# Kernel tuning notes

Hardware: AMD Instinct MI355X
Metric: run time of the kernel (lower is better)

Reference implementation:

```python
import jax, jax.numpy as jnp
import numpy as np

B, N, D, H, DH, F, L, LC = 32, 256, 512, 8, 64, 2048, 8, 2
NEG = -1e9
SCALE = 1.0 / float(np.sqrt(DH))


def _ln(x, g, b, eps=1e-3):
    # keras LayerNormalization default epsilon=1e-3
    m = jnp.mean(x, -1, keepdims=True)
    v = jnp.mean((x - m) ** 2, -1, keepdims=True)
    return (x - m) * jax.lax.rsqrt(v + eps) * g + b


def setup_inputs() -> dict:
    key = jax.random.key(0)
    ks = jax.random.split(key, 20)
    n = lambda k, s: jax.random.normal(k, s, dtype=jnp.float32) * 0.02
    lengths = jax.random.randint(ks[0], (B,), N // 2, N + 1)
    mask = jnp.arange(N)[None, :] < lengths[:, None]  # [B,N] bool
    return {
        'x': jax.random.normal(ks[1], (B, N, D), dtype=jnp.float32),
        'interaction': jax.random.normal(ks[2], (B, N, N, H), dtype=jnp.float32) * 0.1,
        'class_token': n(ks[3], (1, 1, D)),
        'p_ln1_g': jnp.ones((L, D)), 'p_ln1_b': jnp.zeros((L, D)),
        'p_wq': n(ks[4], (L, D, D)), 'p_wk': n(ks[5], (L, D, D)),
        'p_wv': n(ks[6], (L, D, D)), 'p_wo': n(ks[7], (L, D, D)),
        'p_ln2_g': jnp.ones((L, D)), 'p_ln2_b': jnp.zeros((L, D)),
        'p_w1': n(ks[8], (L, D, F)), 'p_b1': jnp.zeros((L, F)),
        'p_w2': n(ks[9], (L, F, D)), 'p_b2': jnp.zeros((L, D)),
        'c_ln1_g': jnp.ones((LC, D)), 'c_ln1_b': jnp.zeros((LC, D)),
        'c_qk': n(ks[10], (LC, D, H, DH)), 'c_qb': jnp.zeros((LC, H, DH)),
        'c_kk': n(ks[11], (LC, D, H, DH)), 'c_kb': jnp.zeros((LC, H, DH)),
        'c_vk': n(ks[12], (LC, D, H, DH)), 'c_vb': jnp.zeros((LC, H, DH)),
        'c_ok': n(ks[13], (LC, H, DH, D)), 'c_ob': jnp.zeros((LC, D)),
        'c_ln2_g': jnp.ones((LC, D)), 'c_ln2_b': jnp.zeros((LC, D)),
        'c_w1': n(ks[14], (LC, D, F)), 'c_b1': jnp.zeros((LC, F)),
        'c_w2': n(ks[15], (LC, F, D)), 'c_b2': jnp.zeros((LC, D)),
        'mask': mask,
    }


def _part_forward(x, interaction, class_token, p_ln1_g, p_ln1_b, p_wq, p_wk, p_wv, p_wo,
                  p_ln2_g, p_ln2_b, p_w1, p_b1, p_w2, p_b2,
                  c_ln1_g, c_ln1_b, c_qk, c_qb, c_kk, c_kb, c_vk, c_vb, c_ok, c_ob,
                  c_ln2_g, c_ln2_b, c_w1, c_b1, c_w2, c_b2, mask):
    # pairwise particle mask [B,1,N,N]; keras Softmax adds (1-mask)*-1e9
    pmask = (mask[:, None, None, :] & mask[:, None, :, None]).astype(x.dtype)
    padd = (1.0 - pmask) * NEG
    inter = jnp.transpose(interaction, (0, 3, 1, 2))  # [B,H,N,N]
    h = x
    for i in range(L):
        # pre-LN interaction self-attention (dropout inactive at inference)
        hn = _ln(h, p_ln1_g[i], p_ln1_b[i])
        q = (hn @ p_wq[i]).reshape(B, N, H, DH)
        k = (hn @ p_wk[i]).reshape(B, N, H, DH)
        v = (hn @ p_wv[i]).reshape(B, N, H, DH)
        s = jnp.einsum('bqhd,bkhd->bhqk', q, k) * SCALE + inter + padd
        a = jax.nn.softmax(s, axis=-1)
        o = jnp.einsum('bhqk,bkhd->bqhd', a, v).reshape(B, N, D) @ p_wo[i]
        h = h + o
        # pre-LN FFN, gelu (exact, tf.nn.gelu default)
        fn = _ln(h, p_ln2_g[i], p_ln2_b[i])
        h = h + (jax.nn.gelu(fn @ p_w1[i] + p_b1[i], approximate=False) @ p_w2[i] + p_b2[i])
    query = jnp.broadcast_to(class_token, (B, 1, D)).astype(x.dtype)
    cmask = jnp.concatenate([jnp.ones((B, 1), bool), mask], axis=1)[:, None, None, :].astype(x.dtype)
    cadd = (1.0 - cmask) * NEG  # [B,1,1,N+1]
    for i in range(LC):
        # class-attention: K/V from LN(concat([token, particles])), Q from RAW token (as in source)
        cat = jnp.concatenate([query, h], axis=1)  # [B,N+1,D]
        cn = _ln(cat, c_ln1_g[i], c_ln1_b[i])
        qh = jnp.einsum('bqd,dhk->bqhk', query, c_qk[i]) + c_qb[i]
        kh = jnp.einsum('bsd,dhk->bshk', cn, c_kk[i]) + c_kb[i]
        vh = jnp.einsum('bsd,dhk->bshk', cn, c_vk[i]) + c_vb[i]
        s = jnp.einsum('bqhk,bshk->bhqs', qh, kh) * SCALE + cadd
        a = jax.nn.softmax(s, axis=-1)
        o = jnp.einsum('bhqs,bshk->bqhk', a, vh)
        o = jnp.einsum('bqhk,hkd->bqd', o, c_ok[i]) + c_ob[i]
        query = query + o
        fn = _ln(query, c_ln2_g[i], c_ln2_b[i])
        query = query + (jax.nn.gelu(fn @ c_w1[i] + c_b1[i], approximate=False) @ c_w2[i] + c_b2[i])
    return query  # [B,1,D]


def reference(x, interaction, class_token, p_ln1_g, p_ln1_b, p_wq, p_wk, p_wv, p_wo,
              p_ln2_g, p_ln2_b, p_w1, p_b1, p_w2, p_b2,
              c_ln1_g, c_ln1_b, c_qk, c_qb, c_kk, c_kb, c_vk, c_vb, c_ok, c_ob,
              c_ln2_g, c_ln2_b, c_w1, c_b1, c_w2, c_b2, mask):
    return _part_forward(x, interaction, class_token, p_ln1_g, p_ln1_b, p_wq, p_wk, p_wv, p_wo,
                         p_ln2_g, p_ln2_b, p_w1, p_b1, p_w2, p_b2,
                         c_ln1_g, c_ln1_b, c_qk, c_qb, c_kk, c_kb, c_vk, c_vb, c_ok, c_ob,
                         c_ln2_g, c_ln2_b, c_w1, c_b1, c_w2, c_b2, mask)
```

## Files before the change

kernel.cpp:

```cpp
#include <hip/hip_runtime.h>
#include <hip/hip_fp16.h>

#define B_ 32
#define N_ 256
#define D_ 512
#define H_ 8
#define DH_ 64
#define F_ 2048
#define L_ 8
#define LC_ 2
#define NEG_ (-1e9f)
#define SCALE_ 0.125f
#define LDSK 72
#define KCH_ 128

typedef unsigned short u16;
typedef unsigned int u32;
typedef long long s64;
typedef __attribute__((ext_vector_type(8))) short bf16x8;
typedef __attribute__((ext_vector_type(8))) unsigned short u16x8;
typedef __attribute__((ext_vector_type(4))) float f32x4;

__device__ __forceinline__ float b2f(u16 u) {
    union { u32 i; float f; } v; v.i = ((u32)u) << 16; return v.f;
}
__device__ __forceinline__ u16 f2b(float f) {
    union { float f; u32 i; } v; v.f = f;
    u32 x = v.i;
    u32 r = (x + 0x7FFFu + ((x >> 16) & 1u)) >> 16;
    return (u16)r;
}
__device__ __forceinline__ float h2f(u16 u) {
    __half_raw hr; hr.x = u;
    return __half2float(__half(hr));
}
__device__ __forceinline__ void gld16(u16* lds, const u16* g) {
    __builtin_amdgcn_global_load_lds(
        (const __attribute__((address_space(1))) u16*)g,
        (__attribute__((address_space(3))) u16*)lds, 16, 0, 0);
}
__device__ __forceinline__ float ldf(const void* p, size_t i, int fl) {
    if (fl == 1) return ((const float*)p)[i];
    if (fl == 0) return b2f(((const u16*)p)[i]);
    return h2f(((const u16*)p)[i]);
}
__device__ __forceinline__ void ld4(const void* p, size_t i, int fl, float o[4]) {
    if (fl == 1) {
        const float4 v = *(const float4*)((const float*)p + i);
        o[0] = v.x; o[1] = v.y; o[2] = v.z; o[3] = v.w;
    } else if (fl == 0) {
        const ushort4 v = *(const ushort4*)((const u16*)p + i);
        o[0] = b2f(v.x); o[1] = b2f(v.y); o[2] = b2f(v.z); o[3] = b2f(v.w);
    } else {
        const ushort4 v = *(const ushort4*)((const u16*)p + i);
        o[0] = h2f(v.x); o[1] = h2f(v.y); o[2] = h2f(v.z); o[3] = h2f(v.w);
    }
}

__global__ void sniff_kernel(const u32* __restrict__ g1, int* __restrict__ flag) {
    if (threadIdx.x == 0 && blockIdx.x == 0) {
        u32 w = g1[0];
        int f = 0;
        if (w == 0x3F800000u) f = 1;
        else if (w == 0x3C003C00u) f = 2;
        flag[0] = f;
    }
}

__global__ void mask_decode_kernel(const unsigned char* __restrict__ raw,
                                   float* __restrict__ mf) {
    int i = blockIdx.x * 256 + threadIdx.x;
    if (i >= B_ * N_) return;
    unsigned char c0 = raw[0], c1 = raw[1], c4 = raw[4];
    bool v;
    if (c1 == 0x3F || c1 == 0x3C) {
        v = ((const u16*)raw)[i] != 0;
    } else if (c0 == 1 && c1 == 1) {
        v = raw[i] != 0;
    } else if (c0 == 1 && c1 == 0) {
        if (c4 == 1) v = ((const int*)raw)[i] != 0;
        else v = ((const long long*)raw)[i] != 0;
    } else {
        v = ((const float*)raw)[i] != 0.0f;
    }
    mf[i] = v ? 1.0f : 0.0f;
}

__global__ void cvt_in_kernel(const void* __restrict__ in, float* __restrict__ out,
                              int n, const int* __restrict__ fl) {
    int i = blockIdx.x * 256 + threadIdx.x;
    if (i < n) out[i] = ldf(in, (size_t)i, fl[0]);
}
__global__ void bcast_token_kernel(const void* __restrict__ ct, float* __restrict__ qry,
                                   const int* __restrict__ fl) {
    int i = blockIdx.x * 256 + threadIdx.x;
    qry[i] = ldf(ct, (size_t)(i & (D_ - 1)), fl[0]);
}
__global__ void out_copy_kernel(const float* __restrict__ in, float* __restrict__ out, int n) {
    int i = blockIdx.x * 256 + threadIdx.x;
    if (i < n) out[i] = in[i];
}
__global__ void concat_bias_kernel(const void* __restrict__ b1, s64 o1,
                                   const void* __restrict__ b2, s64 o2,
                                   float* __restrict__ dst, const int* __restrict__ flp) {
    int i = blockIdx.x * 256 + threadIdx.x;
    if (i < 512) dst[i] = ldf(b1, (size_t)(o1 + i), flp[0]);
    else if (i < 1024) dst[i] = ldf(b2, (size_t)(o2 + i - 512), flp[0]);
}

__global__ __launch_bounds__(256) void inter_t_kernel(const void* __restrict__ inter,
                                                      const float* __restrict__ mf,
                                                      u16* __restrict__ out,
                                                      const int* __restrict__ flp) {
    __shared__ float tile[256][9];
    __shared__ float mks[256];
    int fl = flp[0];
    int bq = blockIdx.x;
    int b = bq >> 8, q = bq & 255;
    int t = threadIdx.x;
    size_t base = (size_t)bq * 2048;
#pragma unroll
    for (int p = 0; p < 8; ++p) {
        int e = p * 256 + t;
        tile[e >> 3][e & 7] = ldf(inter, base + e, fl);
    }
    mks[t] = mf[b * 256 + t];
    __syncthreads();
    float mq = mf[b * 256 + q];
    int h = t >> 5;
    int k0 = (t & 31) * 8;
    u16x8 v8;
#pragma unroll
    for (int ii = 0; ii < 8; ++ii) {
        int k = k0 + ii;
        float v = tile[k][h];
        if (mq * mks[k] < 0.5f) v += NEG_;
        v8[ii] = (short)f2b(v);
    }
    *(u16x8*)(out + (((size_t)(b * 8 + h) * 256 + q) * 256 + k0)) = v8;
}

__global__ __launch_bounds__(256) void transpose_w_kernel(const void* __restrict__ W, s64 weoff,
                                                          int Nst, int Kd,
                                                          u16* __restrict__ wt,
                                                          const int* __restrict__ flp) {
    __shared__ float tile[32][33];
    int fl = flp[0];
    int n0 = blockIdx.x * 32, k0 = blockIdx.y * 32;
    int tr = threadIdx.x >> 5, tc = threadIdx.x & 31;
#pragma unroll
    for (int p = 0; p < 4; ++p) {
        int kk = p * 8 + tr;
        tile[kk][tc] = ldf(W, (size_t)(weoff + (s64)(k0 + kk) * Nst + n0 + tc), fl);
    }
    __syncthreads();
#pragma unroll
    for (int p = 0; p < 4; ++p) {
        int nn = p * 8 + tr;
        wt[(s64)(n0 + nn) * Kd + k0 + tc] = f2b(tile[tc][nn]);
    }
}

__global__ __launch_bounds__(256) void twt6_kernel(const void* __restrict__ wq,
                                                   const void* __restrict__ wk,
                                                   const void* __restrict__ wv,
                                                   const void* __restrict__ wo,
                                                   const void* __restrict__ w1,
                                                   const void* __restrict__ w2,
                                                   s64 off44, s64 offw1, s64 offw2,
                                                   u16* __restrict__ wtqkv,
                                                   u16* __restrict__ wto,
                                                   u16* __restrict__ wt1,
                                                   u16* __restrict__ wt2,
                                                   const int* __restrict__ flp) {
    __shared__ float tile[32][33];
    int fl = flp[0];
    int bid = blockIdx.x;
    const void* W; s64 weoff; int Nst, Kd; u16* dst; int lb;
    if (bid < 256)       { W = wq; weoff = off44; Nst = 512;  Kd = 512;  dst = wtqkv;          lb = bid; }
    else if (bid < 512)  { W = wk; weoff = off44; Nst = 512;  Kd = 512;  dst = wtqkv + 262144; lb = bid - 256; }
    else if (bid < 768)  { W = wv; weoff = off44; Nst = 512;  Kd = 512;  dst = wtqkv + 524288; lb = bid - 512; }
    else if (bid < 1024) { W = wo; weoff = off44; Nst = 512;  Kd = 512;  dst = wto;            lb = bid - 768; }
    else if (bid < 2048) { W = w1; weoff = offw1; Nst = 2048; Kd = 512;  dst = wt1;            lb = bid - 1024; }
    else                 { W = w2; weoff = offw2; Nst = 512;  Kd = 2048; dst = wt2;            lb = bid - 2048; }
    int nx = Nst >> 5;
    int n0 = (lb % nx) << 5, k0 = (lb / nx) << 5;
    int tr = threadIdx.x >> 5, tc = threadIdx.x & 31;
#pragma unroll
    for (int p = 0; p < 4; ++p) {
        int kk = p * 8 + tr;
        tile[kk][tc] = ldf(W, (size_t)(weoff + (s64)(k0 + kk) * Nst + n0 + tc), fl);
    }
    __syncthreads();
#pragma unroll
    for (int p = 0; p < 4; ++p) {
        int nn = p * 8 + tr;
        dst[(s64)(n0 + nn) * Kd + k0 + tc] = f2b(tile[tc][nn]);
    }
}

__global__ __launch_bounds__(256) void ln_kernel(const float* __restrict__ in,
                                                 const void* __restrict__ g,
                                                 const void* __restrict__ bta,
                                                 s64 peoff,
                                                 u16* __restrict__ out,
                                                 const int* __restrict__ flp) {
    __shared__ float ws4[4];
    __shared__ float wsq[4];
    int fl = flp[0];
    size_t row = blockIdx.x;
    int t = threadIdx.x;
    float x0 = in[row * D_ + t];
    float x1 = in[row * D_ + 256 + t];
    float s = x0 + x1;
#pragma unroll
    for (int off = 32; off > 0; off >>= 1) s += __shfl_xor(s, off);
    if ((t & 63) == 0) ws4[t >> 6] = s;
    __syncthreads();
    float mean = (ws4[0] + ws4[1] + ws4[2] + ws4[3]) * (1.0f / D_);
    float d0 = x0 - mean, d1 = x1 - mean;
    float sq = d0 * d0 + d1 * d1;
#pragma unroll
    for (int off = 32; off > 0; off >>= 1) sq += __shfl_xor(sq, off);
    if ((t & 63) == 0) wsq[t >> 6] = sq;
    __syncthreads();
    float var = (wsq[0] + wsq[1] + wsq[2] + wsq[3]) * (1.0f / D_);
    float inv = 1.0f / sqrtf(var + 1e-3f);
    out[row * D_ + t]       = f2b(d0 * inv * ldf(g, peoff + t, fl)       + ldf(bta, peoff + t, fl));
    out[row * D_ + 256 + t] = f2b(d1 * inv * ldf(g, peoff + 256 + t, fl) + ldf(bta, peoff + 256 + t, fl));
}

__global__ __launch_bounds__(256) void ln_cat_kernel(const float* __restrict__ qry,
                                                     const float* __restrict__ h,
                                                     const void* __restrict__ g,
                                                     const void* __restrict__ bta,
                                                     s64 peoff,
                                                     u16* __restrict__ out,
                                                     const int* __restrict__ flp) {
    __shared__ float ws4[4];
    __shared__ float wsq[4];
    int fl = flp[0];
    size_t row = blockIdx.x;
    int b = (int)(row / 257);
    int r = (int)(row % 257);
    const float* src = (r == 0) ? (qry + (size_t)b * D_)
                                : (h + ((size_t)b * N_ + (r - 1)) * D_);
    int t = threadIdx.x;
    float x0 = src[t];
    float x1 = src[256 + t];
    float s = x0 + x1;
#pragma unroll
    for (int off = 32; off > 0; off >>= 1) s += __shfl_xor(s, off);
    if ((t & 63) == 0) ws4[t >> 6] = s;
    __syncthreads();
    float mean = (ws4[0] + ws4[1] + ws4[2] + ws4[3]) * (1.0f / D_);
    float d0 = x0 - mean, d1 = x1 - mean;
    float sq = d0 * d0 + d1 * d1;
#pragma unroll
    for (int off = 32; off > 0; off >>= 1) sq += __shfl_xor(sq, off);
    if ((t & 63) == 0) wsq[t >> 6] = sq;
    __syncthreads();
    float var = (wsq[0] + wsq[1] + wsq[2] + wsq[3]) * (1.0f / D_);
    float inv = 1.0f / sqrtf(var + 1e-3f);
    out[row * D_ + t]       = f2b(d0 * inv * ldf(g, peoff + t, fl)       + ldf(bta, peoff + t, fl));
    out[row * D_ + 256 + t] = f2b(d1 * inv * ldf(g, peoff + 256 + t, fl) + ldf(bta, peoff + 256 + t, fl));
}

__global__ __launch_bounds__(512) void mfma_gemm_t(const u16* __restrict__ A,
                                                   const u16* __restrict__ Wt,
                                                   int wst, int wkoff,
                                                   const void* __restrict__ bias, s64 beoff,
                                                   int bflag,
                                                   const float* __restrict__ res,
                                                   void* __restrict__ C, int cbf,
                                                   int M, int N, int K, int act,
                                                   const int* __restrict__ flp) {
    __shared__ u16 Alds[2 * 128 * 64];
    __shared__ u16 Blds[2 * 128 * 64];
    int tid = threadIdx.x;
    int gx = gridDim.x;
    int nwg = gx * gridDim.y;
    int orig = blockIdx.y * gx + blockIdx.x;
    int xcd = orig & 7;
    int qq = nwg >> 3, rr = nwg & 7;
    int wg = (xcd < rr ? xcd * (qq + 1) : rr * (qq + 1) + (xcd - rr) * qq) + (orig >> 3);
    int bx = wg % gx, by = wg / gx;
    int bm = by << 7, bn = bx << 7;
    int wid = tid >> 6, lane = tid & 63;
    int wm = (wid >> 2) << 6, wn = (wid & 3) << 5;
    int l15 = lane & 15, q = lane >> 4;
    f32x4 acc[4][2];
#pragma unroll
    for (int a = 0; a < 4; ++a)
#pragma unroll
        for (int b = 0; b < 2; ++b) acc[a][b] = (f32x4){0.f, 0.f, 0.f, 0.f};
    int srow = tid >> 3;
    int sseg = tid & 7;
    int xseg = sseg ^ (srow & 7);
    const u16* arow[2];
#pragma unroll
    for (int p = 0; p < 2; ++p) {
        int gr = bm + p * 64 + srow;
        if (gr >= M) gr = M - 1;
        arow[p] = A + (size_t)gr * K + (xseg << 3);
    }
    const u16* brow[2];
#pragma unroll
    for (int p = 0; p < 2; ++p)
        brow[p] = Wt + (size_t)(bn + p * 64 + srow) * wst + wkoff + (xseg << 3);
    int dstoff = srow * 64 + (sseg << 3);
    auto stage = [&](int buf, int k0) {
        u16* Ab = Alds + buf * 8192;
        u16* Bb = Blds + buf * 8192;
#pragma unroll
        for (int p = 0; p < 2; ++p) gld16(&Ab[dstoff + p * 4096], arow[p] + k0);
#pragma unroll
        for (int p = 0; p < 2; ++p) gld16(&Bb[dstoff + p * 4096], brow[p] + k0);
    };
    int nt = K >> 6;
    stage(0, 0);
    if (nt > 1) stage(1, 64);
    for (int t = 0; t < nt; ++t) {
        if (t + 1 < nt) asm volatile("s_waitcnt vmcnt(4)" ::: "memory");
        else            asm volatile("s_waitcnt vmcnt(0)" ::: "memory");
        __builtin_amdgcn_s_barrier();
        asm volatile("" ::: "memory");
        const u16* Ac = Alds + (t & 1) * 8192;
        const u16* Bc = Blds + (t & 1) * 8192;
#pragma unroll
        for (int ks = 0; ks < 2; ++ks) {
            int seg = ((ks * 4 + q) ^ (l15 & 7)) << 3;
            bf16x8 af[4], bfr[2];
#pragma unroll
            for (int mt = 0; mt < 4; ++mt)
                af[mt] = *(const bf16x8*)(&Ac[(wm + mt * 16 + l15) * 64 + seg]);
#pragma unroll
            for (int nt2 = 0; nt2 < 2; ++nt2)
                bfr[nt2] = *(const bf16x8*)(&Bc[(wn + nt2 * 16 + l15) * 64 + seg]);
#pragma unroll
            for (int mt = 0; mt < 4; ++mt)
#pragma unroll
                for (int nt2 = 0; nt2 < 2; ++nt2)
                    acc[mt][nt2] = __builtin_amdgcn_mfma_f32_16x16x32_bf16(
                        af[mt], bfr[nt2], acc[mt][nt2], 0, 0, 0);
        }
        asm volatile("" ::: "memory");
        __builtin_amdgcn_s_barrier();
        if (t + 2 < nt) stage(t & 1, (t + 2) << 6);
    }
    int fl = (bflag >= 0) ? bflag : flp[0];
#pragma unroll
    for (int nt2 = 0; nt2 < 2; ++nt2) {
        int col = bn + wn + nt2 * 16 + l15;
        float bv = bias ? ldf(bias, (size_t)(beoff + col), fl) : 0.f;
#pragma unroll
        for (int mt = 0; mt < 4; ++mt) {
#pragma unroll
            for (int i = 0; i < 4; ++i) {
                int row = bm + wm + mt * 16 + q * 4 + i;
                if (row >= M) continue;
                float c = acc[mt][nt2][i] + bv;
                if (act) c = 0.5f * c * (1.0f + erff(c * 0.70710678118654752f));
                if (res) c += res[(size_t)row * N + col];
                if (cbf) ((u16*)C)[(size_t)row * N + col] = f2b(c);
                else     ((float*)C)[(size_t)row * N + col] = c;
            }
        }
    }
}

__global__ __launch_bounds__(256) void skinny_gemm_kernel(const void* __restrict__ A, int abf,
                                                          const void* __restrict__ W, s64 weoff,
                                                          int wst,
                                                          float* __restrict__ Cp,
                                                          int N, int K,
                                                          const int* __restrict__ flp) {
    __shared__ float As[32 * KCH_];
    int wfl = flp[0];
    int tid = threadIdx.x;
    int bn = blockIdx.x << 6;
    int ks = blockIdx.y;
    int k0 = ks * KCH_;
#pragma unroll
    for (int p = 0; p < (32 * KCH_) / 1024; ++p) {
        int idx = p * 1024 + tid * 4;
        int m = idx >> 7, c = idx & (KCH_ - 1);
        size_t gi = (size_t)m * K + k0 + c;
        if (abf) {
            const ushort4 v = *(const ushort4*)((const u16*)A + gi);
            As[idx]     = b2f(v.x);
            As[idx + 1] = b2f(v.y);
            As[idx + 2] = b2f(v.z);
            As[idx + 3] = b2f(v.w);
        } else {
            *(float4*)&As[idx] = *(const float4*)((const float*)A + gi);
        }
    }
    __syncthreads();
    int tx = tid & 63, ty = tid >> 6;
    int n = bn + tx;
    float acc[8] = {0.f, 0.f, 0.f, 0.f, 0.f, 0.f, 0.f, 0.f};
#pragma unroll 4
    for (int kk = 0; kk < KCH_; kk += 4) {
        float w0 = ldf(W, (size_t)(weoff + (s64)(k0 + kk) * wst + n), wfl);
        float w1 = ldf(W, (size_t)(weoff + (s64)(k0 + kk + 1) * wst + n), wfl);
        float w2 = ldf(W, (size_t)(weoff + (s64)(k0 + kk + 2) * wst + n), wfl);
        float w3 = ldf(W, (size_t)(weoff + (s64)(k0 + kk + 3) * wst + n), wfl);
#pragma unroll
        for (int r = 0; r < 8; ++r) {
            const float4 a = *(const float4*)&As[(ty * 8 + r) * KCH_ + kk];
            acc[r] += a.x * w0 + a.y * w1 + a.z * w2 + a.w * w3;
        }
    }
#pragma unroll
    for (int r = 0; r < 8; ++r)
        Cp[((size_t)ks * 32 + ty * 8 + r) * N + n] = acc[r];
}

__global__ __launch_bounds__(256) void skinny_epi_kernel(const float* __restrict__ Cp,
                                                         int KS, int N,
                                                         const void* __restrict__ bias, s64 beoff,
                                                         const float* __restrict__ res,
                                                         float* __restrict__ C, int act,
                                                         const int* __restrict__ flp) {
    int i = blockIdx.x * 256 + threadIdx.x;
    if (i >= 32 * N) return;
    int n = i % N;
    float s = 0.f;
    for (int ks = 0; ks < KS; ++ks) s += Cp[(size_t)ks * 32 * N + i];
    if (bias) s += ldf(bias, (size_t)(beoff + n), flp[0]);
    if (act) s = 0.5f * s * (1.0f + erff(s * 0.70710678118654752f));
    if (res) s += res[i];
    C[i] = s;
}

__global__ __launch_bounds__(256) void attn_mfma_kernel(const u16* __restrict__ QKV,
                                                        const u16* __restrict__ IT,
                                                        u16* __restrict__ O) {
    __shared__ u16 KV[256 * 72];
    __shared__ u16 Amat[64 * 264];
    int li = blockIdx.y * 4 + blockIdx.x;
    int slot = li >> 3;
    int bh = (li & 7) * 32 + (slot >> 2);
    int q0 = (slot & 3) << 6;
    int b = bh >> 3, hh = bh & 7;
    int tid = threadIdx.x;
    int w = tid >> 6, l = tid & 63, q2 = l >> 4, l15 = l & 15;
    int qrow = q0 + (w << 4) + l15;
    const u16* qptr = QKV + (size_t)(b * N_ + qrow) * 1536 + hh * DH_ + (q2 << 3);
    bf16x8 aq0 = *(const bf16x8*)(qptr);
    bf16x8 aq1 = *(const bf16x8*)(qptr + 32);
    {
        int r = tid >> 3, seg = (tid & 7) << 3;
#pragma unroll
        for (int p = 0; p < 8; ++p) {
            int k = p * 32 + r;
            *(u16x8*)(&KV[k * LDSK + seg]) =
                *(const u16x8*)(QKV + (size_t)(b * N_ + k) * 1536 + 512 + hh * DH_ + seg);
        }
    }
    u16x8 vreg[8];
    {
        const u16* vptr = QKV + (size_t)(b * N_ + (w << 6)) * 1536 + 1024 + hh * DH_ + l;
#pragma unroll
        for (int s = 0; s < 8; ++s)
#pragma unroll
            for (int e = 0; e < 8; ++e)
                vreg[s][e] = vptr[(size_t)(s * 8 + e) * 1536];
    }
    const u16* itp = IT + ((size_t)bh * N_ + q0 + (w << 4) + (q2 << 2)) * N_ + l15;
    u16 itv0[16], itv1[16], itv2[16], itv3[16];
#pragma unroll
    for (int t = 0; t < 16; ++t) {
        itv0[t] = itp[t * 16];
        itv1[t] = itp[(size_t)N_ + t * 16];
        itv2[t] = itp[(size_t)2 * N_ + t * 16];
        itv3[t] = itp[(size_t)3 * N_ + t * 16];
    }
    asm volatile("s_waitcnt lgkmcnt(0)" ::: "memory");
    __builtin_amdgcn_s_barrier();
    __builtin_amdgcn_sched_barrier(0);
    f32x4 acc[16];
#pragma unroll
    for (int t = 0; t < 16; ++t) {
        const u16* kp = &KV[(t * 16 + l15) * LDSK + (q2 << 3)];
        bf16x8 b0 = *(const bf16x8*)(kp);
        bf16x8 b1 = *(const bf16x8*)(kp + 32);
        f32x4 z = (f32x4){0.f, 0.f, 0.f, 0.f};
        z = __builtin_amdgcn_mfma_f32_16x16x32_bf16(aq0, b0, z, 0, 0, 0);
        acc[t] = __builtin_amdgcn_mfma_f32_16x16x32_bf16(aq1, b1, z, 0, 0, 0);
    }
    asm volatile("s_waitcnt lgkmcnt(0)" ::: "memory");
    __builtin_amdgcn_s_barrier();
    __builtin_amdgcn_sched_barrier(0);
#pragma unroll
    for (int s = 0; s < 8; ++s)
        *(u16x8*)(&KV[l * 264 + (w << 6) + s * 8]) = vreg[s];
    float mx[4] = {-3e38f, -3e38f, -3e38f, -3e38f};
#pragma unroll
    for (int t = 0; t < 16; ++t) {
        float s0 = acc[t][0] * SCALE_ + b2f(itv0[t]);
        float s1 = acc[t][1] * SCALE_ + b2f(itv1[t]);
        float s2 = acc[t][2] * SCALE_ + b2f(itv2[t]);
        float s3 = acc[t][3] * SCALE_ + b2f(itv3[t]);
        acc[t][0] = s0; acc[t][1] = s1; acc[t][2] = s2; acc[t][3] = s3;
        mx[0] = fmaxf(mx[0], s0);
        mx[1] = fmaxf(mx[1], s1);
        mx[2] = fmaxf(mx[2], s2);
        mx[3] = fmaxf(mx[3], s3);
    }
#pragma unroll
    for (int i = 0; i < 4; ++i) {
        mx[i] = fmaxf(mx[i], __shfl_xor(mx[i], 1));
        mx[i] = fmaxf(mx[i], __shfl_xor(mx[i], 2));
        mx[i] = fmaxf(mx[i], __shfl_xor(mx[i], 4));
        mx[i] = fmaxf(mx[i], __shfl_xor(mx[i], 8));
    }
    float sum[4] = {0.f, 0.f, 0.f, 0.f};
#pragma unroll
    for (int t = 0; t < 16; ++t)
#pragma unroll
        for (int i = 0; i < 4; ++i) {
            float e = expf(acc[t][i] - mx[i]);
            acc[t][i] = e;
            sum[i] += e;
        }
#pragma unroll
    for (int i = 0; i < 4; ++i) {
        sum[i] += __shfl_xor(sum[i], 1);
        sum[i] += __shfl_xor(sum[i], 2);
        sum[i] += __shfl_xor(sum[i], 4);
        sum[i] += __shfl_xor(sum[i], 8);
        sum[i] = 1.0f / sum[i];
    }
#pragma unroll
    for (int t = 0; t < 16; ++t)
#pragma unroll
        for (int i = 0; i < 4; ++i)
            Amat[((w << 4) + (q2 << 2) + i) * 264 + t * 16 + l15] = f2b(acc[t][i] * sum[i]);
    asm volatile("s_waitcnt lgkmcnt(0)" ::: "memory");
    __builtin_amdgcn_s_barrier();
    __builtin_amdgcn_sched_barrier(0);
    f32x4 pacc[4];
#pragma unroll
    for (int dt = 0; dt < 4; ++dt) pacc[dt] = (f32x4){0.f, 0.f, 0.f, 0.f};
#pragma unroll
    for (int kc = 0; kc < 8; ++kc) {
        bf16x8 af = *(const bf16x8*)(&Amat[((w << 4) + l15) * 264 + kc * 32 + (q2 << 3)]);
#pragma unroll
        for (int dt = 0; dt < 4; ++dt) {
            bf16x8 bf = *(const bf16x8*)(&KV[(dt * 16 + l15) * 264 + kc * 32 + (q2 << 3)]);
            pacc[dt] = __builtin_amdgcn_mfma_f32_16x16x32_bf16(af, bf, pacc[dt], 0, 0, 0);
        }
    }
    u16* ob = O + (size_t)(b * N_ + q0 + (w << 4) + (q2 << 2)) * D_ + hh * DH_ + l15;
#pragma unroll
    for (int dt = 0; dt < 4; ++dt)
#pragma unroll
        for (int i = 0; i < 4; ++i)
            ob[(size_t)i * D_ + dt * 16] = f2b(pacc[dt][i]);
}

__global__ __launch_bounds__(256) void cls_attn_kernel(const float* __restrict__ qh,
                                                       const u16* __restrict__ kvh,
                                                       const float* __restrict__ mf,
                                                       float* __restrict__ O) {
    __shared__ float qs[64];
    __shared__ float am[257];
    __shared__ float wred[4];
    __shared__ float vred[256];
    int b = blockIdx.x >> 3, hh = blockIdx.x & 7;
    int t = threadIdx.x;
    int w = t >> 6, l = t & 63;
    if (t < 64) qs[t] = qh[(size_t)b * D_ + hh * DH_ + t];
    __syncthreads();
    const u16* krow = kvh + (size_t)(b * 257 + t) * 1024 + hh * DH_;
    float s = 0.f;
#pragma unroll
    for (int seg = 0; seg < 8; ++seg) {
        u16x8 kv8 = *(const u16x8*)(krow + seg * 8);
#pragma unroll
        for (int e = 0; e < 8; ++e) s += qs[seg * 8 + e] * b2f(kv8[e]);
    }
    float cm = (t == 0) ? 1.0f : mf[b * N_ + t - 1];
    s = s * SCALE_ + ((cm > 0.5f) ? 0.0f : NEG_);
    float s256 = -1e30f;
    if (t == 0) {
        const u16* krow2 = kvh + (size_t)(b * 257 + 256) * 1024 + hh * DH_;
        float s2 = 0.f;
#pragma unroll
        for (int seg = 0; seg < 8; ++seg) {
            u16x8 kv8 = *(const u16x8*)(krow2 + seg * 8);
#pragma unroll
            for (int e = 0; e < 8; ++e) s2 += qs[seg * 8 + e] * b2f(kv8[e]);
        }
        float cm2 = mf[b * N_ + 255];
        s256 = s2 * SCALE_ + ((cm2 > 0.5f) ? 0.0f : NEG_);
    }
    float mx = (t == 0) ? fmaxf(s, s256) : s;
#pragma unroll
    for (int off = 32; off > 0; off >>= 1) mx = fmaxf(mx, __shfl_xor(mx, off));
    if (l == 0) wred[w] = mx;
    __syncthreads();
    mx = fmaxf(fmaxf(wred[0], wred[1]), fmaxf(wred[2], wred[3]));
    float p = expf(s - mx);
    float p256 = (t == 0) ? expf(s256 - mx) : 0.f;
    float sum = p + p256;
#pragma unroll
    for (int off = 32; off > 0; off >>= 1) sum += __shfl_xor(sum, off);
    __syncthreads();
    if (l == 0) wred[w] = sum;
    __syncthreads();
    float invs = 1.0f / (wred[0] + wred[1] + wred[2] + wred[3]);
    am[t] = p * invs;
    if (t == 0) am[256] = p256 * invs;
    __syncthreads();
    int g = w, d = l;
    const u16* vcol = kvh + (size_t)(b * 257 + g * 64) * 1024 + 512 + hh * DH_ + d;
    float acc = 0.f;
#pragma unroll 8
    for (int j = 0; j < 64; ++j)
        acc += am[g * 64 + j] * b2f(vcol[(size_t)j * 1024]);
    if (g == 3)
        acc += am[256] * b2f(kvh[(size_t)(b * 257 + 256) * 1024 + 512 + hh * DH_ + d]);
    vred[t] = acc;
    __syncthreads();
    if (t < 64)
        O[(size_t)b * D_ + hh * DH_ + t] = vred[t] + vred[64 + t] + vred[128 + t] + vred[192 + t];
}

extern "C" void kernel_launch(void* const* d_in, const int* in_sizes, int n_in,
                              void* d_out, int out_size, void* d_ws, size_t ws_size,
                              hipStream_t stream) {
    const void* x           = d_in[0];
    const void* interaction = d_in[1];
    const void* class_token = d_in[2];
    const void* p_ln1_g = d_in[3];
    const void* p_ln1_b = d_in[4];
    const void* p_wq    = d_in[5];
    const void* p_wk    = d_in[6];
    const void* p_wv    = d_in[7];
    const void* p_wo    = d_in[8];
    const void* p_ln2_g = d_in[9];
    const void* p_ln2_b = d_in[10];
    const void* p_w1    = d_in[11];
    const void* p_b1    = d_in[12];
    const void* p_w2    = d_in[13];
    const void* p_b2    = d_in[14];
    const void* c_ln1_g = d_in[15];
    const void* c_ln1_b = d_in[16];
    const void* c_qk    = d_in[17];
    const void* c_qb    = d_in[18];
    const void* c_kk    = d_in[19];
    const void* c_kb    = d_in[20];
    const void* c_vk    = d_in[21];
    const void* c_vb    = d_in[22];
    const void* c_ok    = d_in[23];
    const void* c_ob    = d_in[24];
    const void* c_ln2_g = d_in[25];
    const void* c_ln2_b = d_in[26];
    const void* c_w1    = d_in[27];
    const void* c_b1    = d_in[28];
    const void* c_w2    = d_in[29];
    const void* c_b2    = d_in[30];
    const unsigned char* maskraw = (const unsigned char*)d_in[31];

    const size_t NT  = (size_t)B_ * N_;
    const size_t NTD = NT * D_;

    char* base = (char*)d_ws;
    int*   flag   = (int*)base;
    float* maskf  = (float*)(base + 64);
    float* h      = (float*)(base + 64 + 32768);
    u16*   hn     = (u16*)(h + NTD);
    u16*   qkv    = hn + (size_t)B_ * 257 * D_;
    float* qry    = (float*)(qkv + (size_t)8192 * 1536);
    float* qh     = qry + 16384;
    float* ocls   = qh + 16384;
    u16*   fnq    = (u16*)(ocls + 16384);
    float* midc   = (float*)(fnq + 16384);
    float* biaskv = midc + 65536;
    u16*   wt     = (u16*)(biaskv + 1024);
    u16*   wtqkv = wt;
    u16*   wto   = wt + 786432;
    u16*   wt1   = wt + 1048576;
    u16*   wt2   = wt + 2097152;
    u16*   inter_t = wt + 3145728;
    u16*   midfull = inter_t + (size_t)B_ * H_ * N_ * N_;
    float* cpart = (float*)(qkv + (size_t)8224 * 1024);

    auto mgemm = [&](const u16* A, const u16* Wt, int wst, int wkoff,
                     const void* bias, s64 beoff, int bflag, const float* res, void* C, int cbf,
                     int M, int N, int K, int act) {
        dim3 grid(N / 128, (M + 127) / 128);
        mfma_gemm_t<<<grid, 512, 0, stream>>>(A, Wt, wst, wkoff, bias, beoff, bflag,
                                              res, C, cbf, M, N, K, act, flag);
    };
    auto skgemm = [&](const void* A, int abf, const void* W, s64 weoff, int wst,
                      const void* bias, s64 beoff, const float* res, float* C,
                      int N, int K, int act) {
        int KS = K / KCH_;
        skinny_gemm_kernel<<<dim3(N / 64, KS), 256, 0, stream>>>(A, abf, W, weoff, wst,
                                                                 cpart, N, K, flag);
        skinny_epi_kernel<<<(32 * N + 255) / 256, 256, 0, stream>>>(cpart, KS, N, bias, beoff,
                                                                    res, C, act, flag);
    };
    auto twt = [&](const void* W, s64 weoff, int Nst, int Kd, u16* dst) {
        dim3 grid(Nst / 32, Kd / 32);
        transpose_w_kernel<<<grid, 256, 0, stream>>>(W, weoff, Nst, Kd, dst, flag);
    };

    sniff_kernel<<<1, 64, 0, stream>>>((const u32*)p_ln1_g, flag);
    mask_decode_kernel<<<32, 256, 0, stream>>>(maskraw, maskf);
    inter_t_kernel<<<8192, 256, 0, stream>>>(interaction, maskf, inter_t, flag);
    cvt_in_kernel<<<(int)(NTD / 256), 256, 0, stream>>>(x, h, (int)NTD, flag);
    bcast_token_kernel<<<64, 256, 0, stream>>>(class_token, qry, flag);

    for (int i = 0; i < L_; ++i) {
        s64 wo = (s64)i * D_ * D_;
        twt6_kernel<<<3072, 256, 0, stream>>>(p_wq, p_wk, p_wv, p_wo, p_w1, p_w2,
                                              wo, (s64)i * D_ * F_, (s64)i * F_ * D_,
                                              wtqkv, wto, wt1, wt2, flag);
        ln_kernel<<<(int)NT, 256, 0, stream>>>(h, p_ln1_g, p_ln1_b, (s64)i * D_, hn, flag);
        mgemm(hn, wtqkv, D_, 0, nullptr, 0, -1, nullptr, qkv, 1, (int)NT, 1536, D_, 0);
        attn_mfma_kernel<<<dim3(4, B_ * H_), 256, 0, stream>>>(qkv, inter_t, hn);
        mgemm(hn, wto, D_, 0, nullptr, 0, -1, h, h, 0, (int)NT, D_, D_, 0);
        ln_kernel<<<(int)NT, 256, 0, stream>>>(h, p_ln2_g, p_ln2_b, (s64)i * D_, hn, flag);
        mgemm(hn, wt1, D_, 0, p_b1, (s64)i * F_, -1, nullptr, midfull, 1,
              (int)NT, 2048, D_, 1);
        mgemm(midfull, wt2, F_, 0, p_b2, (s64)i * D_, -1, h, h, 0,
              (int)NT, D_, F_, 0);
    }

    for (int i = 0; i < LC_; ++i) {
        s64 wo = (s64)i * D_ * D_;
        twt(c_kk, wo, D_, D_, wtqkv);
        twt(c_vk, wo, D_, D_, wtqkv + 262144);
        concat_bias_kernel<<<4, 256, 0, stream>>>(c_kb, (s64)i * D_, c_vb, (s64)i * D_, biaskv, flag);
        ln_cat_kernel<<<B_ * 257, 256, 0, stream>>>(qry, h, c_ln1_g, c_ln1_b, (s64)i * D_, hn, flag);
        skgemm(qry, 0, c_qk, wo, D_, c_qb, (s64)i * D_, nullptr, qh, D_, D_, 0);
        mgemm(hn, wtqkv, D_, 0, biaskv, 0, 1, nullptr, qkv, 1, B_ * 257, 1024, D_, 0);
        cls_attn_kernel<<<B_ * H_, 256, 0, stream>>>(qh, qkv, maskf, ocls);
        skgemm(ocls, 0, c_ok, wo, D_, c_ob, (s64)i * D_, qry, qry, D_, D_, 0);
        ln_kernel<<<B_, 256, 0, stream>>>(qry, c_ln2_g, c_ln2_b, (s64)i * D_, fnq, flag);
        skgemm(fnq, 1, c_w1, (s64)i * D_ * F_, F_, c_b1, (s64)i * F_, nullptr, midc, F_, D_, 1);
        skgemm(midc, 0, c_w2, (s64)i * F_ * D_, D_, c_b2, (s64)i * D_, qry, qry, D_, F_, 0);
    }

    out_copy_kernel<<<(out_size + 255) / 256, 256, 0, stream>>>(qry, (float*)d_out, out_size);
}
```

Measured before the change: 2.138 ms.

## Transpose all layer weights in one upfront kernel; one-wave-per-row vectorized layernorm

Replaces the per-layer weight transpose/convert launches (8 part layers plus the class-attention K/V transposes) with a single large kernel that converts every layer's weights into a dedicated bf16 buffer before the layer loop. Each layer then indexes its own slice instead of re-transposing into a shared scratch buffer. LayerNorm kernels are rewritten so one 64-lane wave handles a whole row with float4 loads and a packed 8-element bf16 store, removing shared memory and block barriers, with four rows per block. This trades extra workspace for all transposed weights for fewer launches and serialization between the transposes and the GEMMs.

```diff
diff --git a/kernel.cpp b/kernel.cpp
--- a/kernel.cpp
+++ b/kernel.cpp
@@ -140,49 +140,41 @@
     *(u16x8*)(out + (((size_t)(b * 8 + h) * 256 + q) * 256 + k0)) = v8;
 }
 
-__global__ __launch_bounds__(256) void transpose_w_kernel(const void* __restrict__ W, s64 weoff,
-                                                          int Nst, int Kd,
-                                                          u16* __restrict__ wt,
-                                                          const int* __restrict__ flp) {
-    __shared__ float tile[32][33];
-    int fl = flp[0];
-    int n0 = blockIdx.x * 32, k0 = blockIdx.y * 32;
-    int tr = threadIdx.x >> 5, tc = threadIdx.x & 31;
-#pragma unroll
-    for (int p = 0; p < 4; ++p) {
-        int kk = p * 8 + tr;
-        tile[kk][tc] = ldf(W, (size_t)(weoff + (s64)(k0 + kk) * Nst + n0 + tc), fl);
-    }
-    __syncthreads();
-#pragma unroll
-    for (int p = 0; p < 4; ++p) {
-        int nn = p * 8 + tr;
-        wt[(s64)(n0 + nn) * Kd + k0 + tc] = f2b(tile[tc][nn]);
-    }
-}
-
-__global__ __launch_bounds__(256) void twt6_kernel(const void* __restrict__ wq,
-                                                   const void* __restrict__ wk,
-                                                   const void* __restrict__ wv,
-                                                   const void* __restrict__ wo,
-                                                   const void* __restrict__ w1,
-                                                   const void* __restrict__ w2,
-                                                   s64 off44, s64 offw1, s64 offw2,
-                                                   u16* __restrict__ wtqkv,
-                                                   u16* __restrict__ wto,
-                                                   u16* __restrict__ wt1,
-                                                   u16* __restrict__ wt2,
-                                                   const int* __restrict__ flp) {
+__global__ __launch_bounds__(256) void twt_all_kernel(const void* __restrict__ wq,
+                                                      const void* __restrict__ wk,
+                                                      const void* __restrict__ wv,
+                                                      const void* __restrict__ wo,
+                                                      const void* __restrict__ w1,
+                                                      const void* __restrict__ w2,
+                                                      const void* __restrict__ ckk,
+                                                      const void* __restrict__ cvk,
+                                                      u16* __restrict__ wtall,
+                                                      u16* __restrict__ ctall,
+                                                      const int* __restrict__ flp) {
     __shared__ float tile[32][33];
     int fl = flp[0];
     int bid = blockIdx.x;
     const void* W; s64 weoff; int Nst, Kd; u16* dst; int lb;
-    if (bid < 256)       { W = wq; weoff = off44; Nst = 512;  Kd = 512;  dst = wtqkv;          lb = bid; }
-    else if (bid < 512)  { W = wk; weoff = off44; Nst = 512;  Kd = 512;  dst = wtqkv + 262144; lb = bid - 256; }
-    else if (bid < 768)  { W = wv; weoff = off44; Nst = 512;  Kd = 512;  dst = wtqkv + 524288; lb = bid - 512; }
-    else if (bid < 1024) { W = wo; weoff = off44; Nst = 512;  Kd = 512;  dst = wto;            lb = bid - 768; }
-    else if (bid < 2048) { W = w1; weoff = offw1; Nst = 2048; Kd = 512;  dst = wt1;            lb = bid - 1024; }
-    else                 { W = w2; weoff = offw2; Nst = 512;  Kd = 2048; dst = wt2;            lb = bid - 2048; }
+    if (bid < 24576) {
+        int layer = bid / 3072, slot = bid - layer * 3072;
+        s64 off44 = (s64)layer * 512 * 512;
+        u16* base = wtall + (size_t)layer * 3145728;
+        if (slot < 256)       { W = wq; weoff = off44; Nst = 512;  Kd = 512;  dst = base;           lb = slot; }
+        else if (slot < 512)  { W = wk; weoff = off44; Nst = 512;  Kd = 512;  dst = base + 262144;  lb = slot - 256; }
+        else if (slot < 768)  { W = wv; weoff = off44; Nst = 512;  Kd = 512;  dst = base + 524288;  lb = slot - 512; }
+        else if (slot < 1024) { W = wo; weoff = off44; Nst = 512;  Kd = 512;  dst = base + 786432;  lb = slot - 768; }
+        else if (slot < 2048) { W = w1; weoff = (s64)layer * 512 * 2048; Nst = 2048; Kd = 512;
+                                dst = base + 1048576; lb = slot - 1024; }
+        else                  { W = w2; weoff = (s64)layer * 2048 * 512; Nst = 512;  Kd = 2048;
+                                dst = base + 2097152; lb = slot - 2048; }
+    } else {
+        int cb = bid - 24576;
+        int layer = cb >> 9, slot = cb & 511;
+        weoff = (s64)layer * 512 * 512; Nst = 512; Kd = 512;
+        W = (slot < 256) ? ckk : cvk;
+        dst = ctall + (size_t)layer * 524288 + ((slot < 256) ? 0 : 262144);
+        lb = slot & 255;
+    }
     int nx = Nst >> 5;
     int n0 = (lb % nx) << 5, k0 = (lb / nx) << 5;
     int tr = threadIdx.x >> 5, tc = threadIdx.x & 31;
@@ -205,29 +197,33 @@
                                                  s64 peoff,
                                                  u16* __restrict__ out,
                                                  const int* __restrict__ flp) {
-    __shared__ float ws4[4];
-    __shared__ float wsq[4];
     int fl = flp[0];
-    size_t row = blockIdx.x;
-    int t = threadIdx.x;
-    float x0 = in[row * D_ + t];
-    float x1 = in[row * D_ + 256 + t];
-    float s = x0 + x1;
+    size_t row = (size_t)blockIdx.x * 4 + (threadIdx.x >> 6);
+    int l = threadIdx.x & 63;
+    const float* src = in + row * D_ + l * 8;
+    float4 x0 = *(const float4*)(src);
+    float4 x1 = *(const float4*)(src + 4);
+    float s = x0.x + x0.y + x0.z + x0.w + x1.x + x1.y + x1.z + x1.w;
 #pragma unroll
     for (int off = 32; off > 0; off >>= 1) s += __shfl_xor(s, off);
-    if ((t & 63) == 0) ws4[t >> 6] = s;
-    __syncthreads();
-    float mean = (ws4[0] + ws4[1] + ws4[2] + ws4[3]) * (1.0f / D_);
-    float d0 = x0 - mean, d1 = x1 - mean;
-    float sq = d0 * d0 + d1 * d1;
+    float mean = s * (1.0f / D_);
+    float d[8] = {x0.x - mean, x0.y - mean, x0.z - mean, x0.w - mean,
+                  x1.x - mean, x1.y - mean, x1.z - mean, x1.w - mean};
+    float sq = 0.f;
+#pragma unroll
+    for (int e = 0; e < 8; ++e) sq += d[e] * d[e];
 #pragma unroll
     for (int off = 32; off > 0; off >>= 1) sq += __shfl_xor(sq, off);
-    if ((t & 63) == 0) wsq[t >> 6] = sq;
-    __syncthreads();
-    float var = (wsq[0] + wsq[1] + wsq[2] + wsq[3]) * (1.0f / D_);
-    float inv = 1.0f / sqrtf(var + 1e-3f);
-    out[row * D_ + t]       = f2b(d0 * inv * ldf(g, peoff + t, fl)       + ldf(bta, peoff + t, fl));
-    out[row * D_ + 256 + t] = f2b(d1 * inv * ldf(g, peoff + 256 + t, fl) + ldf(bta, peoff + 256 + t, fl));
+    float inv = 1.0f / sqrtf(sq * (1.0f / D_) + 1e-3f);
+    float gv[8], bv[8];
+    ld4(g, (size_t)(peoff + l * 8), fl, gv);
+    ld4(g, (size_t)(peoff + l * 8 + 4), fl, gv + 4);
+    ld4(bta, (size_t)(peoff + l * 8), fl, bv);
+    ld4(bta, (size_t)(peoff + l * 8 + 4), fl, bv + 4);
+    u16x8 o8;
+#pragma unroll
+    for (int e = 0; e < 8; ++e) o8[e] = f2b(d[e] * inv * gv[e] + bv[e]);
+    *(u16x8*)(out + row * D_ + l * 8) = o8;
 }
 
 __global__ __launch_bounds__(256) void ln_cat_kernel(const float* __restrict__ qry,
@@ -237,33 +233,36 @@
                                                      s64 peoff,
                                                      u16* __restrict__ out,
                                                      const int* __restrict__ flp) {
-    __shared__ float ws4[4];
-    __shared__ float wsq[4];
     int fl = flp[0];
-    size_t row = blockIdx.x;
+    size_t row = (size_t)blockIdx.x * 4 + (threadIdx.x >> 6);
+    int l = threadIdx.x & 63;
     int b = (int)(row / 257);
     int r = (int)(row % 257);
-    const float* src = (r == 0) ? (qry + (size_t)b * D_)
-                                : (h + ((size_t)b * N_ + (r - 1)) * D_);
-    int t = threadIdx.x;
-    float x0 = src[t];
-    float x1 = src[256 + t];
-    float s = x0 + x1;
+    const float* src = ((r == 0) ? (qry + (size_t)b * D_)
+                                 : (h + ((size_t)b * N_ + (r - 1)) * D_)) + l * 8;
+    float4 x0 = *(const float4*)(src);
+    float4 x1 = *(const float4*)(src + 4);
+    float s = x0.x + x0.y + x0.z + x0.w + x1.x + x1.y + x1.z + x1.w;
 #pragma unroll
     for (int off = 32; off > 0; off >>= 1) s += __shfl_xor(s, off);
-    if ((t & 63) == 0) ws4[t >> 6] = s;
-    __syncthreads();
-    float mean = (ws4[0] + ws4[1] + ws4[2] + ws4[3]) * (1.0f / D_);
-    float d0 = x0 - mean, d1 = x1 - mean;
-    float sq = d0 * d0 + d1 * d1;
+    float mean = s * (1.0f / D_);
+    float d[8] = {x0.x - mean, x0.y - mean, x0.z - mean, x0.w - mean,
+                  x1.x - mean, x1.y - mean, x1.z - mean, x1.w - mean};
+    float sq = 0.f;
+#pragma unroll
+    for (int e = 0; e < 8; ++e) sq += d[e] * d[e];
 #pragma unroll
     for (int off = 32; off > 0; off >>= 1) sq += __shfl_xor(sq, off);
-    if ((t & 63) == 0) wsq[t >> 6] = sq;
-    __syncthreads();
-    float var = (wsq[0] + wsq[1] + wsq[2] + wsq[3]) * (1.0f / D_);
-    float inv = 1.0f / sqrtf(var + 1e-3f);
-    out[row * D_ + t]       = f2b(d0 * inv * ldf(g, peoff + t, fl)       + ldf(bta, peoff + t, fl));
-    out[row * D_ + 256 + t] = f2b(d1 * inv * ldf(g, peoff + 256 + t, fl) + ldf(bta, peoff + 256 + t, fl));
+    float inv = 1.0f / sqrtf(sq * (1.0f / D_) + 1e-3f);
+    float gv[8], bv[8];
+    ld4(g, (size_t)(peoff + l * 8), fl, gv);
+    ld4(g, (size_t)(peoff + l * 8 + 4), fl, gv + 4);
+    ld4(bta, (size_t)(peoff + l * 8), fl, bv);
+    ld4(bta, (size_t)(peoff + l * 8 + 4), fl, bv + 4);
+    u16x8 o8;
+#pragma unroll
+    for (int e = 0; e < 8; ++e) o8[e] = f2b(d[e] * inv * gv[e] + bv[e]);
+    *(u16x8*)(out + row * D_ + l * 8) = o8;
 }
 
 __global__ __launch_bounds__(512) void mfma_gemm_t(const u16* __restrict__ A,
@@ -680,13 +679,11 @@
     u16*   fnq    = (u16*)(ocls + 16384);
     float* midc   = (float*)(fnq + 16384);
     float* biaskv = midc + 65536;
-    u16*   wt     = (u16*)(biaskv + 1024);
-    u16*   wtqkv = wt;
-    u16*   wto   = wt + 786432;
-    u16*   wt1   = wt + 1048576;
-    u16*   wt2   = wt + 2097152;
-    u16*   inter_t = wt + 3145728;
+    u16*   spare  = (u16*)(biaskv + 1024);
+    u16*   inter_t = spare + 3145728;
     u16*   midfull = inter_t + (size_t)B_ * H_ * N_ * N_;
+    u16*   wtall   = midfull + (size_t)8192 * 2048;
+    u16*   ctall   = wtall + (size_t)8 * 3145728;
     float* cpart = (float*)(qkv + (size_t)8224 * 1024);
 
     auto mgemm = [&](const u16* A, const u16* Wt, int wst, int wkoff,
@@ -705,27 +702,25 @@
         skinny_epi_kernel<<<(32 * N + 255) / 256, 256, 0, stream>>>(cpart, KS, N, bias, beoff,
                                                                     res, C, act, flag);
     };
-    auto twt = [&](const void* W, s64 weoff, int Nst, int Kd, u16* dst) {
-        dim3 grid(Nst / 32, Kd / 32);
-        transpose_w_kernel<<<grid, 256, 0, stream>>>(W, weoff, Nst, Kd, dst, flag);
-    };
 
     sniff_kernel<<<1, 64, 0, stream>>>((const u32*)p_ln1_g, flag);
     mask_decode_kernel<<<32, 256, 0, stream>>>(maskraw, maskf);
+    twt_all_kernel<<<25600, 256, 0, stream>>>(p_wq, p_wk, p_wv, p_wo, p_w1, p_w2,
+                                              c_kk, c_vk, wtall, ctall, flag);
     inter_t_kernel<<<8192, 256, 0, stream>>>(interaction, maskf, inter_t, flag);
     cvt_in_kernel<<<(int)(NTD / 256), 256, 0, stream>>>(x, h, (int)NTD, flag);
     bcast_token_kernel<<<64, 256, 0, stream>>>(class_token, qry, flag);
 
     for (int i = 0; i < L_; ++i) {
-        s64 wo = (s64)i * D_ * D_;
-        twt6_kernel<<<3072, 256, 0, stream>>>(p_wq, p_wk, p_wv, p_wo, p_w1, p_w2,
-                                              wo, (s64)i * D_ * F_, (s64)i * F_ * D_,
-                                              wtqkv, wto, wt1, wt2, flag);
-        ln_kernel<<<(int)NT, 256, 0, stream>>>(h, p_ln1_g, p_ln1_b, (s64)i * D_, hn, flag);
+        u16* wtqkv = wtall + (size_t)i * 3145728;
+        u16* wto   = wtqkv + 786432;
+        u16* wt1   = wtqkv + 1048576;
+        u16* wt2   = wtqkv + 2097152;
+        ln_kernel<<<(int)(NT / 4), 256, 0, stream>>>(h, p_ln1_g, p_ln1_b, (s64)i * D_, hn, flag);
         mgemm(hn, wtqkv, D_, 0, nullptr, 0, -1, nullptr, qkv, 1, (int)NT, 1536, D_, 0);
         attn_mfma_kernel<<<dim3(4, B_ * H_), 256, 0, stream>>>(qkv, inter_t, hn);
         mgemm(hn, wto, D_, 0, nullptr, 0, -1, h, h, 0, (int)NT, D_, D_, 0);
-        ln_kernel<<<(int)NT, 256, 0, stream>>>(h, p_ln2_g, p_ln2_b, (s64)i * D_, hn, flag);
+        ln_kernel<<<(int)(NT / 4), 256, 0, stream>>>(h, p_ln2_g, p_ln2_b, (s64)i * D_, hn, flag);
         mgemm(hn, wt1, D_, 0, p_b1, (s64)i * F_, -1, nullptr, midfull, 1,
               (int)NT, 2048, D_, 1);
         mgemm(midfull, wt2, F_, 0, p_b2, (s64)i * D_, -1, h, h, 0,
@@ -734,15 +729,14 @@
 
     for (int i = 0; i < LC_; ++i) {
         s64 wo = (s64)i * D_ * D_;
-        twt(c_kk, wo, D_, D_, wtqkv);
-        twt(c_vk, wo, D_, D_, wtqkv + 262144);
+        u16* kvw = ctall + (size_t)i * 524288;
         concat_bias_kernel<<<4, 256, 0, stream>>>(c_kb, (s64)i * D_, c_vb, (s64)i * D_, biaskv, flag);
-        ln_cat_kernel<<<B_ * 257, 256, 0, stream>>>(qry, h, c_ln1_g, c_ln1_b, (s64)i * D_, hn, flag);
+        ln_cat_kernel<<<2056, 256, 0, stream>>>(qry, h, c_ln1_g, c_ln1_b, (s64)i * D_, hn, flag);
         skgemm(qry, 0, c_qk, wo, D_, c_qb, (s64)i * D_, nullptr, qh, D_, D_, 0);
-        mgemm(hn, wtqkv, D_, 0, biaskv, 0, 1, nullptr, qkv, 1, B_ * 257, 1024, D_, 0);
+        mgemm(hn, kvw, D_, 0, biaskv, 0, 1, nullptr, qkv, 1, B_ * 257, 1024, D_, 0);
         cls_attn_kernel<<<B_ * H_, 256, 0, stream>>>(qh, qkv, maskf, ocls);
         skgemm(ocls, 0, c_ok, wo, D_, c_ob, (s64)i * D_, qry, qry, D_, D_, 0);
-        ln_kernel<<<B_, 256, 0, stream>>>(qry, c_ln2_g, c_ln2_b, (s64)i * D_, fnq, flag);
+        ln_kernel<<<8, 256, 0, stream>>>(qry, c_ln2_g, c_ln2_b, (s64)i * D_, fnq, flag);
         skgemm(fnq, 1, c_w1, (s64)i * D_ * F_, F_, c_b1, (s64)i * F_, nullptr, midc, F_, D_, 1);
         skgemm(midc, 0, c_w2, (s64)i * F_ * D_, D_, c_b2, (s64)i * D_, qry, qry, D_, F_, 0);
     }
```

New measurement: 2.033 ms. 4.9% less time.
